# Kernel optimization log

Hardware: AMD Instinct MI355X
Metric: run time of the kernel (lower is better)

Reference implementation:

```python
import jax, jax.numpy as jnp
import numpy as np
from jax import lax

N, E, H = 100000, 768, 1024   # candidates, span-emb dim, FFNN hidden
K, A = 1500, 50               # top-k mentions, max antecedents
NUM_DOCS = 10

def _ffnn(x, w0, b0, w1, b1, w2, b2):
    h = jax.nn.relu(x @ w0 + b0)
    h = jax.nn.relu(h @ w1 + b1)
    return (h @ w2 + b2)[..., 0]

def setup_inputs() -> dict:
    key = jax.random.key(0)
    ks = jax.random.split(key, 8)
    emb = jax.random.normal(ks[0], (N, E), dtype=jnp.float32)
    doc_ids = jnp.sort(jax.random.randint(ks[1], (N,), 0, NUM_DOCS))
    def w(k, shape):
        fan_in = shape[0]
        return jax.random.normal(k, shape, dtype=jnp.float32) / np.sqrt(fan_in)
    return {
        'candidate_span_emb': emb,
        'candidate_doc_ids': doc_ids,
        'uw0': w(ks[2], (E, H)), 'ub0': jnp.zeros((H,), jnp.float32),
        'uw1': w(ks[3], (H, H)), 'ub1': jnp.zeros((H,), jnp.float32),
        'uw2': w(ks[4], (H, 1)), 'ub2': jnp.zeros((1,), jnp.float32),
        'pw0': w(ks[5], (3 * E, H)), 'pb0': jnp.zeros((H,), jnp.float32),
        'pw1': w(ks[6], (H, H)), 'pb1': jnp.zeros((H,), jnp.float32),
        'pw2': w(ks[7], (H, 1)), 'pb2': jnp.zeros((1,), jnp.float32),
    }

def reference(candidate_span_emb, candidate_doc_ids,
              uw0, ub0, uw1, ub1, uw2, ub2,
              pw0, pb0, pw1, pb1, pw2, pb2):
    # 1) unary mention scores over all candidate spans  [N]
    scores = _ffnn(candidate_span_emb, uw0, ub0, uw1, ub1, uw2, ub2)
    # 2) top-k span pruning (extract_spans with sort_spans=True -> sorted ids)
    _, top_idx = lax.top_k(scores, K)
    top_idx = jnp.sort(top_idx)
    mention_emb = candidate_span_emb[top_idx]          # [K, E]
    mention_scores = scores[top_idx]                   # [K]
    mention_doc_ids = candidate_doc_ids[top_idx]       # [K]
    # 3) antecedent index construction + doc-boundary mask
    raw = jnp.arange(K)[:, None] - (jnp.arange(A) + 1)[None, :]   # [K, A]
    antecedents = jnp.maximum(raw, 0)
    mask = (mention_doc_ids[:, None] == mention_doc_ids[antecedents]) & (raw >= 0)
    log_mask = jnp.where(mask, 0.0, -jnp.inf).astype(jnp.float32)
    # 4) pairwise antecedent scoring: [m, a, m*a] -> FFNN + unary terms
    ante_emb = mention_emb[antecedents]                 # [K, A, E]
    tgt = jnp.broadcast_to(mention_emb[:, None, :], (K, A, E))
    pair_emb = jnp.concatenate([tgt, ante_emb, tgt * ante_emb], axis=-1)  # [K, A, 3E]
    pair_scores = _ffnn(pair_emb, pw0, pb0, pw1, pb1, pw2, pb2)           # [K, A]
    ante_scores = pair_scores + mention_scores[:, None] + mention_scores[antecedents]
    # 5) dummy antecedent column prepended
    out = jnp.concatenate([jnp.zeros((K, 1), jnp.float32), ante_scores + log_mask], axis=1)
    return out  # [K, A+1]
```

## Files before the change

### kernel.cpp

```cpp
#include <hip/hip_runtime.h>
#include <cstdint>
#include <cstddef>

#define NC 100000
#define ED 768
#define HD 1024
#define KTOP 1500
#define AA 50
#define NPAIR (KTOP*AA)
#define PSTRIDE 100096
#define PSLICES 8

typedef __attribute__((ext_vector_type(8))) short v8s;
typedef __attribute__((ext_vector_type(4))) float f32x4;

__device__ __forceinline__ float relu_(float x){ return fmaxf(x, 0.f); }
__device__ __forceinline__ float bf2f(ushort h){ return __uint_as_float(((unsigned)h) << 16); }
__device__ __forceinline__ ushort f2b(float f){
    unsigned u = __float_as_uint(f);
    return (ushort)((u + 0x7fffu + ((u >> 16) & 1u)) >> 16);
}
__device__ __forceinline__ unsigned pack2(float a, float b){
    return (unsigned)f2b(a) | ((unsigned)f2b(b) << 16);
}
__device__ __forceinline__ unsigned fkey(float s){
    unsigned u = __float_as_uint(s);
    return (u & 0x80000000u) ? ~u : (u | 0x80000000u);
}
__device__ __forceinline__ float sanitize_(float v)
{
    unsigned bu = __float_as_uint(v);
    if ((bu & 0x7f800000u) == 0x7f800000u)
        v = (bu & 0x007fffffu) ? 0.f : ((bu >> 31) ? -3.0e38f : 3.0e38f);
    return v;
}

#define AS1(p) ((const __attribute__((address_space(1))) void*)(p))
#define AS3(p) ((__attribute__((address_space(3))) void*)(p))

template<int EPI>
__global__ __launch_bounds__(256, 4)
void bgemm_k(const ushort* __restrict__ A, int lda,
             const ushort* __restrict__ BT, int ldb,
             void* __restrict__ Cv, int ldc, int M, int Ksz, int MP,
             const float* __restrict__ bias,
             const float* __restrict__ Ub, const float* __restrict__ Vb, int p0,
             const float* __restrict__ w2, float* __restrict__ partS)
{
    const int bid = blockIdx.x;
    const int xcd = bid & 7;
    const int i0  = bid >> 3;
    const int np  = i0 & 7;
    const int bmp = ((i0 >> 3) << 3) + xcd;
    if (bmp >= MP) return;
    const int bm = bmp << 7;
    const int bn = np << 7;

    __shared__ __align__(16) ushort Al[128*64];
    __shared__ __align__(16) ushort Bl[128*64];
    __shared__ float srow[2][128];
    const int t = threadIdx.x;
    const int l = t & 63;
    const int w = t >> 6;
    const int wr = (w >> 1) << 6;
    const int wc = (w & 1) << 6;
    const int r15 = l & 15, q4 = l >> 4;
    const int srow8 = l >> 3;
    const int schnk = l & 7;

    f32x4 acc[4][4];
#pragma unroll
    for (int r = 0; r < 4; ++r)
#pragma unroll
        for (int c = 0; c < 4; ++c) acc[r][c] = (f32x4){0.f,0.f,0.f,0.f};

    for (int k0 = 0; k0 < Ksz; k0 += 64) {
        __syncthreads();
#pragma unroll
        for (int q = 0; q < 4; ++q) {
            int rbase = w*32 + q*8;
            int row = rbase + srow8;
            int cs = schnk ^ (row & 7);
            int gr = bm + row; if (gr > M-1) gr = M-1;
            __builtin_amdgcn_global_load_lds(AS1(A + (size_t)gr*lda + k0 + cs*8),
                                             AS3(Al + rbase*64), 16, 0, 0);
            int gn = bn + row;
            __builtin_amdgcn_global_load_lds(AS1(BT + (size_t)gn*ldb + k0 + cs*8),
                                             AS3(Bl + rbase*64), 16, 0, 0);
        }
        __syncthreads();
#pragma unroll
        for (int ks = 0; ks < 2; ++ks) {
            const int clin = ks*4 + q4;
            v8s af[4], bf[4];
#pragma unroll
            for (int r = 0; r < 4; ++r) {
                int row = wr + r*16 + r15;
                af[r] = *(const v8s*)(Al + row*64 + ((clin ^ (row & 7))*8));
                int col = wc + r*16 + r15;
                bf[r] = *(const v8s*)(Bl + col*64 + ((clin ^ (col & 7))*8));
            }
#pragma unroll
            for (int r = 0; r < 4; ++r)
#pragma unroll
                for (int c = 0; c < 4; ++c)
                    acc[r][c] = __builtin_amdgcn_mfma_f32_16x16x32_bf16(bf[c], af[r], acc[r][c], 0, 0, 0);
        }
    }

    if (EPI == 4) {
        float sacc[4];
#pragma unroll
        for (int r = 0; r < 4; ++r) sacc[r] = 0.f;
#pragma unroll
        for (int c = 0; c < 4; ++c) {
            int n0 = bn + wc + c*16 + q4*4;
            const float4 bb = *(const float4*)(bias + n0);
            const float4 ww = *(const float4*)(w2 + n0);
#pragma unroll
            for (int r = 0; r < 4; ++r) {
                sacc[r] = fmaf(relu_(acc[r][c][0] + bb.x), ww.x, sacc[r]);
                sacc[r] = fmaf(relu_(acc[r][c][1] + bb.y), ww.y, sacc[r]);
                sacc[r] = fmaf(relu_(acc[r][c][2] + bb.z), ww.z, sacc[r]);
                sacc[r] = fmaf(relu_(acc[r][c][3] + bb.w), ww.w, sacc[r]);
            }
        }
        __syncthreads();
        srow[t >> 7][t & 127] = 0.f;
        __syncthreads();
#pragma unroll
        for (int r = 0; r < 4; ++r) {
            float s = sacc[r];
            s += __shfl_xor(s, 16, 64);
            s += __shfl_xor(s, 32, 64);
            if (q4 == 0) srow[w & 1][wr + r*16 + r15] = s;
        }
        __syncthreads();
        if (t < 128) {
            int m = bm + t;
            if (m < M) partS[(size_t)np*PSTRIDE + m] = srow[0][t] + srow[1][t];
        }
    } else {
        float*  Cf = (float*)Cv;
        ushort* Cb = (ushort*)Cv;
#pragma unroll
        for (int r = 0; r < 4; ++r) {
            int m = bm + wr + r*16 + r15;
            if (m >= M) continue;
            int iu = 0, iv = 0;
            if (EPI == 3) {
                int p = p0 + m;
                iu = p / 50;
                int a = p - iu*50;
                iv = iu - a - 1; if (iv < 0) iv = 0;
            }
#pragma unroll
            for (int c = 0; c < 4; ++c) {
                int n0 = bn + wc + c*16 + q4*4;
                float x0 = acc[r][c][0], x1 = acc[r][c][1];
                float x2 = acc[r][c][2], x3 = acc[r][c][3];
                if (EPI == 0) {
                    float4 o; o.x=x0; o.y=x1; o.z=x2; o.w=x3;
                    *(float4*)(Cf + (size_t)m*ldc + n0) = o;
                } else if (EPI == 1) {
                    const float4 bb = *(const float4*)(bias + n0);
                    float4 o; o.x=x0+bb.x; o.y=x1+bb.y; o.z=x2+bb.z; o.w=x3+bb.w;
                    *(float4*)(Cf + (size_t)m*ldc + n0) = o;
                } else if (EPI == 2) {
                    const float4 bb = *(const float4*)(bias + n0);
                    uint2 o;
                    o.x = pack2(relu_(x0+bb.x), relu_(x1+bb.y));
                    o.y = pack2(relu_(x2+bb.z), relu_(x3+bb.w));
                    *(uint2*)(Cb + (size_t)m*ldc + n0) = o;
                } else {
                    const float4 uu = *(const float4*)(Ub + (size_t)iu*HD + n0);
                    const float4 vv = *(const float4*)(Vb + (size_t)iv*HD + n0);
                    uint2 o;
                    o.x = pack2(relu_(x0+uu.x+vv.x), relu_(x1+uu.y+vv.y));
                    o.y = pack2(relu_(x2+uu.z+vv.z), relu_(x3+uu.w+vv.w));
                    *(uint2*)(Cb + (size_t)m*ldc + n0) = o;
                }
            }
        }
    }
}

__global__ void comb_k(const float* __restrict__ part, const float* __restrict__ b2,
                       float* __restrict__ out, int M)
{
    int i = blockIdx.x*256 + threadIdx.x;
    if (i < M) {
        float s = b2[0];
#pragma unroll
        for (int p = 0; p < PSLICES; ++p) s += part[(size_t)p*PSTRIDE + i];
        out[i] = s;
    }
}

__global__ void conv_k(const float* __restrict__ src, ushort* __restrict__ dst, int n4)
{
    for (int x = blockIdx.x*blockDim.x + threadIdx.x; x < n4; x += gridDim.x*blockDim.x) {
        float4 v = ((const float4*)src)[x];
        ushort4 o; o.x = f2b(v.x); o.y = f2b(v.y); o.z = f2b(v.z); o.w = f2b(v.w);
        ((ushort4*)dst)[x] = o;
    }
}

__global__ __launch_bounds__(256)
void wt_k(const float* __restrict__ W, ushort* __restrict__ WT, int K, int N)
{
    __shared__ float ld[32][33];
    int tx = threadIdx.x & 31, ty = threadIdx.x >> 5;
    int k0 = blockIdx.y*32, n0 = blockIdx.x*32;
#pragma unroll
    for (int r = 0; r < 4; ++r)
        ld[ty + r*8][tx] = W[(size_t)(k0 + ty + r*8)*N + n0 + tx];
    __syncthreads();
#pragma unroll
    for (int r = 0; r < 4; ++r)
        WT[(size_t)(n0 + ty + r*8)*K + k0 + tx] = f2b(ld[tx][ty + r*8]);
}

__global__ void init_sel_k(unsigned* state, unsigned* hist, int* top, int ntop)
{
    int t = threadIdx.x;
    if (t < 64) state[t] = 0u;
    for (int i = t; i < 1024; i += 256) hist[i] = 0u;
    for (int k = t; k < ntop; k += 256) top[k] = k;
}

__global__ __launch_bounds__(256)
void hist_k(const float* __restrict__ scores, int N, unsigned* __restrict__ hist,
            const unsigned* __restrict__ state, int shift)
{
    __shared__ unsigned lh[256];
    lh[threadIdx.x] = 0u;
    __syncthreads();
    unsigned prefix = state[0];
    for (int i = blockIdx.x*blockDim.x + threadIdx.x; i < N; i += gridDim.x*blockDim.x) {
        unsigned u = fkey(scores[i]);
        bool ok = (shift == 24) || ((u >> (shift+8)) == prefix);
        if (ok) atomicAdd(&lh[(u >> shift) & 0xffu], 1u);
    }
    __syncthreads();
    unsigned c = lh[threadIdx.x];
    if (c) atomicAdd(&hist[threadIdx.x], c);
}

__global__ void select_k(const unsigned* __restrict__ hist, unsigned* state, int shift, int K)
{
    if (threadIdx.x != 0) return;
    unsigned P = state[1];
    unsigned acc = 0; int bstar = 0;
    for (int b = 255; b >= 0; --b) {
        unsigned h = hist[b];
        if (P + acc + h >= (unsigned)K) { bstar = b; break; }
        acc += h;
    }
    state[0] = (shift == 24) ? (unsigned)bstar : ((state[0] << 8) | (unsigned)bstar);
    state[1] = P + acc;
    if (shift == 0) state[2] = state[0];
}

__global__ __launch_bounds__(256)
void cnt_k(const float* __restrict__ scores, int N, const unsigned* __restrict__ state,
           unsigned* __restrict__ gt_cnt, unsigned* __restrict__ eq_cnt)
{
    unsigned ut = state[2];
    int base = blockIdx.x * 2048;
    unsigned g = 0, e = 0;
    for (int q = 0; q < 8; ++q) {
        int i = base + q*256 + threadIdx.x;
        if (i < N) { unsigned u = fkey(scores[i]); g += (u > ut); e += (u == ut); }
    }
    __shared__ unsigned sg[256], se[256];
    sg[threadIdx.x] = g; se[threadIdx.x] = e;
    __syncthreads();
    for (int s = 128; s > 0; s >>= 1) {
        if (threadIdx.x < s) { sg[threadIdx.x] += sg[threadIdx.x+s]; se[threadIdx.x] += se[threadIdx.x+s]; }
        __syncthreads();
    }
    if (threadIdx.x == 0) { gt_cnt[blockIdx.x] = sg[0]; eq_cnt[blockIdx.x] = se[0]; }
}

__global__ void scan_k(const unsigned* gt_cnt, const unsigned* eq_cnt,
                       unsigned* gt_off, unsigned* eq_off, int nblk, unsigned* state, int K)
{
    if (threadIdx.x != 0) return;
    unsigned ag = 0, ae = 0;
    for (int b = 0; b < nblk; ++b) {
        gt_off[b] = ag; eq_off[b] = ae;
        ag += gt_cnt[b]; ae += eq_cnt[b];
    }
    state[3] = ag;
    state[4] = ag < (unsigned)K ? (unsigned)K - ag : 0u;
}

__global__ __launch_bounds__(256)
void write_k(const float* __restrict__ scores, int N, const unsigned* __restrict__ state,
             const unsigned* __restrict__ gt_off, const unsigned* __restrict__ eq_off,
             int* __restrict__ top_idx, int Ksel)
{
    unsigned ut = state[2], T = state[4];
    int base = blockIdx.x * 2048;
    unsigned grun = gt_off[blockIdx.x], erun = eq_off[blockIdx.x];
    __shared__ unsigned wg[4], we[4];
    int t = threadIdx.x, lane = t & 63, wv = t >> 6;
    for (int q = 0; q < 8; ++q) {
        int i = base + q*256 + t;
        bool valid = i < N;
        unsigned u = valid ? fkey(scores[i]) : 0u;
        bool g = valid && (u > ut);
        bool e = valid && (u == ut);
        unsigned long long bg = __ballot(g), be = __ballot(e);
        unsigned long long lt = (1ull << lane) - 1ull;
        unsigned lpg = __popcll(bg & lt), lpe = __popcll(be & lt);
        if (lane == 0) { wg[wv] = (unsigned)__popcll(bg); we[wv] = (unsigned)__popcll(be); }
        __syncthreads();
        unsigned bsg = 0, bse = 0, tg = 0, te = 0;
        for (int ww = 0; ww < 4; ++ww) {
            if (ww < wv) { bsg += wg[ww]; bse += we[ww]; }
            tg += wg[ww]; te += we[ww];
        }
        unsigned grank = grun + bsg + lpg;
        unsigned erank = erun + bse + lpe;
        unsigned pos = 0xffffffffu;
        if (g)                   pos = grank + (erank < T ? erank : T);
        else if (e && erank < T) pos = grank + erank;
        if (pos < (unsigned)Ksel) top_idx[pos] = i;
        grun += tg; erun += te;
        __syncthreads();
    }
}

__global__ void gatherF_k(const float* __restrict__ emb, const int* __restrict__ doc,
                          const int* __restrict__ topA, const float* __restrict__ scores,
                          ushort* __restrict__ meb, float* __restrict__ ms,
                          int* __restrict__ mdoc)
{
    int k = blockIdx.x;
    int idx = topA[k]; if (idx < 0 || idx >= NC) idx = 0;
    int t = threadIdx.x;
    if (t < 192) {
        float4 v = ((const float4*)(emb + (size_t)idx*ED))[t];
        ushort4 o; o.x = f2b(v.x); o.y = f2b(v.y); o.z = f2b(v.z); o.w = f2b(v.w);
        *(ushort4*)(meb + (size_t)k*ED + t*4) = o;
    }
    if (t == 192) { ms[k] = scores[idx]; mdoc[k] = doc[idx]; }
}

__global__ __launch_bounds__(256)
void prodb_k(const ushort* __restrict__ meb, ushort* __restrict__ prod, int p0, int C)
{
    int tot = C * 96;
    for (int x = blockIdx.x*blockDim.x + threadIdx.x; x < tot; x += gridDim.x*blockDim.x) {
        int pc = x / 96, e = x - pc*96;
        int p = p0 + pc;
        int i = p / 50, a = p - i*50;
        int j = i - a - 1; if (j < 0) j = 0;
        uint4 ui = ((const uint4*)(meb + (size_t)i*ED))[e];
        uint4 uj = ((const uint4*)(meb + (size_t)j*ED))[e];
        auto pk = [](unsigned a_, unsigned b_) -> unsigned {
            float lo = bf2f((ushort)(a_ & 0xffffu)) * bf2f((ushort)(b_ & 0xffffu));
            float hi = bf2f((ushort)(a_ >> 16))     * bf2f((ushort)(b_ >> 16));
            return (unsigned)f2b(lo) | ((unsigned)f2b(hi) << 16);
        };
        uint4 o; o.x = pk(ui.x, uj.x); o.y = pk(ui.y, uj.y);
                 o.z = pk(ui.z, uj.z); o.w = pk(ui.w, uj.w);
        ((uint4*)(prod + (size_t)pc*ED))[e] = o;
    }
}

__global__ __launch_bounds__(256)
void assemble_k(const float* __restrict__ ps, const float* __restrict__ ms,
                const int* __restrict__ mdoc, float* __restrict__ out)
{
    int idx = blockIdx.x*blockDim.x + threadIdx.x;
    if (idx >= KTOP*(AA+1)) return;
    int i = idx / (AA+1), col = idx - i*(AA+1);
    if (col == 0) { out[idx] = 0.f; return; }
    int a = col - 1;
    int raw = i - a - 1;
    int j = raw < 0 ? 0 : raw;
    bool mk = (raw >= 0) && (mdoc[i] == mdoc[j]);
    float v = mk ? (ps[i*AA + a] + ms[i] + ms[j]) : -3.0e38f;
    out[idx] = sanitize_(v);
}

static inline int swz_grid(int MP) { return ((MP + 7) & ~7) * 8; }

extern "C" void kernel_launch(void* const* d_in, const int* in_sizes, int n_in,
                              void* d_out, int out_size, void* d_ws, size_t ws_size,
                              hipStream_t stream)
{
    const float* emb = (const float*)d_in[0];
    const int*   doc = (const int*)d_in[1];
    const float* uw0 = (const float*)d_in[2];
    const float* ub0 = (const float*)d_in[3];
    const float* uw1 = (const float*)d_in[4];
    const float* ub1 = (const float*)d_in[5];
    const float* uw2 = (const float*)d_in[6];
    const float* ub2 = (const float*)d_in[7];
    const float* pw0 = (const float*)d_in[8];
    const float* pb0 = (const float*)d_in[9];
    const float* pw1 = (const float*)d_in[10];
    const float* pb1 = (const float*)d_in[11];
    const float* pw2 = (const float*)d_in[12];
    const float* pb2 = (const float*)d_in[13];
    float* out = (float*)d_out;

    char* ws = (char*)d_ws;
    size_t off = 0;
    auto alloc = [&](size_t bytes) -> void* {
        void* p = ws + off;
        off = (off + bytes + 255) & ~(size_t)255;
        return p;
    };
    const int NBLKA = (NC + 2047) / 2048;
    float*    scoresA = (float*)alloc((size_t)NC*4);
    float*    partS   = (float*)alloc((size_t)PSLICES*PSTRIDE*4);
    unsigned* stateA  = (unsigned*)alloc(64*4);
    unsigned* histA   = (unsigned*)alloc(1024*4);
    unsigned* gtA  = (unsigned*)alloc((size_t)NBLKA*4);
    unsigned* eqA  = (unsigned*)alloc((size_t)NBLKA*4);
    unsigned* gtoA = (unsigned*)alloc((size_t)NBLKA*4);
    unsigned* eqoA = (unsigned*)alloc((size_t)NBLKA*4);
    int*      topA = (int*)alloc((size_t)KTOP*4);
    ushort*   meb  = (ushort*)alloc((size_t)KTOP*ED*2);
    float*    ms   = (float*)alloc((size_t)KTOP*4);
    int*      mdoc = (int*)alloc((size_t)KTOP*4);
    float*    U    = (float*)alloc((size_t)KTOP*HD*4);
    float*    V    = (float*)alloc((size_t)KTOP*HD*4);
    float*    ps   = (float*)alloc((size_t)NPAIR*4);
    ushort*   uw0T = (ushort*)alloc((size_t)HD*ED*2);
    ushort*   uw1T = (ushort*)alloc((size_t)HD*HD*2);
    ushort*   paT  = (ushort*)alloc((size_t)HD*ED*2);
    ushort*   pbT  = (ushort*)alloc((size_t)HD*ED*2);
    ushort*   pcT  = (ushort*)alloc((size_t)HD*ED*2);
    ushort*   pw1T = (ushort*)alloc((size_t)HD*HD*2);
    size_t fixed = off;
    size_t avail = ws_size > fixed ? ws_size - fixed : 0;

    wt_k<<<dim3(HD/32, ED/32), 256, 0, stream>>>(uw0, uw0T, ED, HD);
    wt_k<<<dim3(HD/32, HD/32), 256, 0, stream>>>(uw1, uw1T, HD, HD);
    wt_k<<<dim3(HD/32, ED/32), 256, 0, stream>>>(pw0, paT, ED, HD);
    wt_k<<<dim3(HD/32, ED/32), 256, 0, stream>>>(pw0 + (size_t)ED*HD, pbT, ED, HD);
    wt_k<<<dim3(HD/32, ED/32), 256, 0, stream>>>(pw0 + (size_t)2*ED*HD, pcT, ED, HD);
    wt_k<<<dim3(HD/32, HD/32), 256, 0, stream>>>(pw1, pw1T, HD, HD);

    {
        long Rl = (long)(avail / 3584);
        int R = (int)(Rl > 100096 ? 100096 : Rl);
        R &= ~127; if (R < 128) R = 128;
        ushort* embB = (ushort*)(ws + fixed);
        ushort* H1b  = embB + (size_t)R*ED;
        for (int r0 = 0; r0 < NC; r0 += R) {
            int rows = NC - r0 < R ? NC - r0 : R;
            int MP = (rows + 127)/128;
            conv_k<<<1024, 256, 0, stream>>>(emb + (size_t)r0*ED, embB, rows*192);
            bgemm_k<2><<<swz_grid(MP), 256, 0, stream>>>(embB, ED, uw0T, ED, H1b, HD,
                rows, ED, MP, ub0, nullptr, nullptr, 0, nullptr, nullptr);
            bgemm_k<4><<<swz_grid(MP), 256, 0, stream>>>(H1b, HD, uw1T, HD, nullptr, 0,
                rows, HD, MP, ub1, nullptr, nullptr, 0, uw2, partS);
            comb_k<<<(rows + 255)/256, 256, 0, stream>>>(partS, ub2, scoresA + r0, rows);
        }
    }

    init_sel_k<<<1, 256, 0, stream>>>(stateA, histA, topA, KTOP);
    for (int pass = 0; pass < 4; ++pass) {
        int shift = 24 - pass*8;
        hist_k<<<256, 256, 0, stream>>>(scoresA, NC, histA + pass*256, stateA, shift);
        select_k<<<1, 64, 0, stream>>>(histA + pass*256, stateA, shift, KTOP);
    }
    cnt_k<<<NBLKA, 256, 0, stream>>>(scoresA, NC, stateA, gtA, eqA);
    scan_k<<<1, 64, 0, stream>>>(gtA, eqA, gtoA, eqoA, NBLKA, stateA, KTOP);
    write_k<<<NBLKA, 256, 0, stream>>>(scoresA, NC, stateA, gtoA, eqoA, topA, KTOP);
    gatherF_k<<<KTOP, 256, 0, stream>>>(emb, doc, topA, scoresA, meb, ms, mdoc);

    {
        int MP = (KTOP + 127)/128;
        bgemm_k<1><<<swz_grid(MP), 256, 0, stream>>>(meb, ED, paT, ED, U, HD, KTOP, ED,
            MP, pb0, nullptr, nullptr, 0, nullptr, nullptr);
        bgemm_k<0><<<swz_grid(MP), 256, 0, stream>>>(meb, ED, pbT, ED, V, HD, KTOP, ED,
            MP, nullptr, nullptr, nullptr, 0, nullptr, nullptr);
    }

    {
        long Cl = (long)(avail / 3584);
        int Cp = (int)(Cl > NPAIR ? NPAIR : Cl);
        Cp &= ~127; if (Cp < 128) Cp = 128;
        ushort* prodb = (ushort*)(ws + fixed);
        ushort* h0b = prodb + (size_t)Cp*ED;
        for (int p0 = 0; p0 < NPAIR; p0 += Cp) {
            int pc = NPAIR - p0 < Cp ? NPAIR - p0 : Cp;
            int MP = (pc + 127)/128;
            prodb_k<<<1024, 256, 0, stream>>>(meb, prodb, p0, pc);
            bgemm_k<3><<<swz_grid(MP), 256, 0, stream>>>(prodb, ED, pcT, ED, h0b, HD,
                pc, ED, MP, nullptr, U, V, p0, nullptr, nullptr);
            bgemm_k<4><<<swz_grid(MP), 256, 0, stream>>>(h0b, HD, pw1T, HD, nullptr, 0,
                pc, HD, MP, pb1, nullptr, nullptr, 0, pw2, partS);
            comb_k<<<(pc + 255)/256, 256, 0, stream>>>(partS, pb2, ps + p0, pc);
        }
    }

    assemble_k<<<(KTOP*(AA+1) + 255)/256, 256, 0, stream>>>(ps, ms, mdoc, out);
}
```

Measured before the change: 1.021 ms.

## Compact valid antecedent pairs and skip FFNN work on masked pairs

Adds a count, scan and write pass that builds a compacted index list of antecedent pairs that are valid: a non-negative antecedent index in the same document. The pair product construction and both pairwise GEMMs then run only over those compacted rows, with the effective row count read on the device. The combine step scatters scores back to their original pair positions. This removes GEMM work for pairs whose output is forced to -inf by the mask. In exchange it adds three small kernels and an indirect index load. Masked score slots are now left unwritten, which is only safe if the assemble step ignores them rather than adding -inf to leftover values.

```diff
diff --git a/kernel.cpp b/kernel.cpp
--- a/kernel.cpp
+++ b/kernel.cpp
@@ -8,6 +8,7 @@
 #define KTOP 1500
 #define AA 50
 #define NPAIR (KTOP*AA)
+#define NBLKP ((NPAIR + 2047) / 2048)
 #define PSTRIDE 100096
 #define PSLICES 8
 
@@ -45,7 +46,8 @@
              void* __restrict__ Cv, int ldc, int M, int Ksz, int MP,
              const float* __restrict__ bias,
              const float* __restrict__ Ub, const float* __restrict__ Vb, int p0,
-             const float* __restrict__ w2, float* __restrict__ partS)
+             const float* __restrict__ w2, float* __restrict__ partS,
+             const int* __restrict__ cntp, const int* __restrict__ pidx)
 {
     const int bid = blockIdx.x;
     const int xcd = bid & 7;
@@ -53,7 +55,14 @@
     const int np  = i0 & 7;
     const int bmp = ((i0 >> 3) << 3) + xcd;
     if (bmp >= MP) return;
+    int Meff = M;
+    if (cntp) {
+        int c = *cntp - p0;
+        if (c < Meff) Meff = c;
+        if (Meff <= 0) return;
+    }
     const int bm = bmp << 7;
+    if (bm >= Meff) return;
     const int bn = np << 7;
 
     __shared__ __align__(16) ushort Al[128*64];
@@ -81,7 +90,7 @@
             int rbase = w*32 + q*8;
             int row = rbase + srow8;
             int cs = schnk ^ (row & 7);
-            int gr = bm + row; if (gr > M-1) gr = M-1;
+            int gr = bm + row; if (gr > Meff-1) gr = Meff-1;
             __builtin_amdgcn_global_load_lds(AS1(A + (size_t)gr*lda + k0 + cs*8),
                                              AS3(Al + rbase*64), 16, 0, 0);
             int gn = bn + row;
@@ -138,7 +147,7 @@
         __syncthreads();
         if (t < 128) {
             int m = bm + t;
-            if (m < M) partS[(size_t)np*PSTRIDE + m] = srow[0][t] + srow[1][t];
+            if (m < Meff) partS[(size_t)np*PSTRIDE + m] = srow[0][t] + srow[1][t];
         }
     } else {
         float*  Cf = (float*)Cv;
@@ -146,10 +155,10 @@
 #pragma unroll
         for (int r = 0; r < 4; ++r) {
             int m = bm + wr + r*16 + r15;
-            if (m >= M) continue;
+            if (m >= Meff) continue;
             int iu = 0, iv = 0;
             if (EPI == 3) {
-                int p = p0 + m;
+                int p = pidx[p0 + m];
                 iu = p / 50;
                 int a = p - iu*50;
                 iv = iu - a - 1; if (iv < 0) iv = 0;
@@ -197,6 +206,20 @@
     }
 }
 
+__global__ void combp_k(const float* __restrict__ part, const float* __restrict__ b2,
+                        float* __restrict__ ps, int Cp, int p0,
+                        const int* __restrict__ cntp, const int* __restrict__ pidx)
+{
+    int i = blockIdx.x*256 + threadIdx.x;
+    int Meff = *cntp - p0; if (Meff > Cp) Meff = Cp;
+    if (i < Meff) {
+        float s = b2[0];
+#pragma unroll
+        for (int p = 0; p < PSLICES; ++p) s += part[(size_t)p*PSTRIDE + i];
+        ps[pidx[p0 + i]] = s;
+    }
+}
+
 __global__ void conv_k(const float* __restrict__ src, ushort* __restrict__ dst, int n4)
 {
     for (int x = blockIdx.x*blockDim.x + threadIdx.x; x < n4; x += gridDim.x*blockDim.x) {
@@ -349,13 +372,78 @@
     if (t == 192) { ms[k] = scores[idx]; mdoc[k] = doc[idx]; }
 }
 
-__global__ __launch_bounds__(256)
-void prodb_k(const ushort* __restrict__ meb, ushort* __restrict__ prod, int p0, int C)
-{
-    int tot = C * 96;
+__device__ __forceinline__ bool pvalid_(int p, const int* __restrict__ mdoc)
+{
+    int i = p / 50, a = p - i*50;
+    int j = i - a - 1;
+    return (j >= 0) && (mdoc[i] == mdoc[j]);
+}
+
+__global__ __launch_bounds__(256)
+void pcnt_k(const int* __restrict__ mdoc, unsigned* __restrict__ blk_cnt)
+{
+    int base = blockIdx.x * 2048;
+    unsigned c = 0;
+    for (int q = 0; q < 8; ++q) {
+        int p = base + q*256 + threadIdx.x;
+        if (p < NPAIR && pvalid_(p, mdoc)) ++c;
+    }
+    __shared__ unsigned sc[256];
+    sc[threadIdx.x] = c;
+    __syncthreads();
+    for (int s = 128; s > 0; s >>= 1) {
+        if (threadIdx.x < s) sc[threadIdx.x] += sc[threadIdx.x + s];
+        __syncthreads();
+    }
+    if (threadIdx.x == 0) blk_cnt[blockIdx.x] = sc[0];
+}
+
+__global__ void pscan_k(const unsigned* __restrict__ blk_cnt,
+                        unsigned* __restrict__ blk_off, int* __restrict__ pcnt)
+{
+    if (threadIdx.x != 0) return;
+    unsigned a = 0;
+    for (int b = 0; b < NBLKP; ++b) { blk_off[b] = a; a += blk_cnt[b]; }
+    pcnt[0] = (int)a;
+}
+
+__global__ __launch_bounds__(256)
+void pwrite_k(const int* __restrict__ mdoc, const unsigned* __restrict__ blk_off,
+              int* __restrict__ pidx)
+{
+    int base = blockIdx.x * 2048;
+    unsigned run = blk_off[blockIdx.x];
+    __shared__ unsigned wcnt[4];
+    int t = threadIdx.x, lane = t & 63, wv = t >> 6;
+    for (int q = 0; q < 8; ++q) {
+        int p = base + q*256 + t;
+        bool v = (p < NPAIR) && pvalid_(p, mdoc);
+        unsigned long long bv = __ballot(v);
+        unsigned long long lt = (1ull << lane) - 1ull;
+        unsigned lp = __popcll(bv & lt);
+        if (lane == 0) wcnt[wv] = (unsigned)__popcll(bv);
+        __syncthreads();
+        unsigned bs = 0, tot = 0;
+        for (int ww = 0; ww < 4; ++ww) {
+            if (ww < wv) bs += wcnt[ww];
+            tot += wcnt[ww];
+        }
+        if (v) pidx[run + bs + lp] = p;
+        run += tot;
+        __syncthreads();
+    }
+}
+
+__global__ __launch_bounds__(256)
+void prodb_k(const ushort* __restrict__ meb, ushort* __restrict__ prod, int p0, int Cp,
+             const int* __restrict__ cntp, const int* __restrict__ pidx)
+{
+    int Meff = *cntp - p0; if (Meff > Cp) Meff = Cp;
+    if (Meff <= 0) return;
+    int tot = Meff * 96;
     for (int x = blockIdx.x*blockDim.x + threadIdx.x; x < tot; x += gridDim.x*blockDim.x) {
         int pc = x / 96, e = x - pc*96;
-        int p = p0 + pc;
+        int p = pidx[p0 + pc];
         int i = p / 50, a = p - i*50;
         int j = i - a - 1; if (j < 0) j = 0;
         uint4 ui = ((const uint4*)(meb + (size_t)i*ED))[e];
@@ -432,6 +520,10 @@
     float*    U    = (float*)alloc((size_t)KTOP*HD*4);
     float*    V    = (float*)alloc((size_t)KTOP*HD*4);
     float*    ps   = (float*)alloc((size_t)NPAIR*4);
+    unsigned* pbc  = (unsigned*)alloc((size_t)NBLKP*4);
+    unsigned* pbo  = (unsigned*)alloc((size_t)NBLKP*4);
+    int*      pcnt = (int*)alloc(256);
+    int*      pidx = (int*)alloc((size_t)NPAIR*4);
     ushort*   uw0T = (ushort*)alloc((size_t)HD*ED*2);
     ushort*   uw1T = (ushort*)alloc((size_t)HD*HD*2);
     ushort*   paT  = (ushort*)alloc((size_t)HD*ED*2);
@@ -459,9 +551,11 @@
             int MP = (rows + 127)/128;
             conv_k<<<1024, 256, 0, stream>>>(emb + (size_t)r0*ED, embB, rows*192);
             bgemm_k<2><<<swz_grid(MP), 256, 0, stream>>>(embB, ED, uw0T, ED, H1b, HD,
-                rows, ED, MP, ub0, nullptr, nullptr, 0, nullptr, nullptr);
+                rows, ED, MP, ub0, nullptr, nullptr, 0, nullptr, nullptr,
+                nullptr, nullptr);
             bgemm_k<4><<<swz_grid(MP), 256, 0, stream>>>(H1b, HD, uw1T, HD, nullptr, 0,
-                rows, HD, MP, ub1, nullptr, nullptr, 0, uw2, partS);
+                rows, HD, MP, ub1, nullptr, nullptr, 0, uw2, partS,
+                nullptr, nullptr);
             comb_k<<<(rows + 255)/256, 256, 0, stream>>>(partS, ub2, scoresA + r0, rows);
         }
     }
@@ -477,12 +571,16 @@
     write_k<<<NBLKA, 256, 0, stream>>>(scoresA, NC, stateA, gtoA, eqoA, topA, KTOP);
     gatherF_k<<<KTOP, 256, 0, stream>>>(emb, doc, topA, scoresA, meb, ms, mdoc);
 
+    pcnt_k<<<NBLKP, 256, 0, stream>>>(mdoc, pbc);
+    pscan_k<<<1, 64, 0, stream>>>(pbc, pbo, pcnt);
+    pwrite_k<<<NBLKP, 256, 0, stream>>>(mdoc, pbo, pidx);
+
     {
         int MP = (KTOP + 127)/128;
         bgemm_k<1><<<swz_grid(MP), 256, 0, stream>>>(meb, ED, paT, ED, U, HD, KTOP, ED,
-            MP, pb0, nullptr, nullptr, 0, nullptr, nullptr);
+            MP, pb0, nullptr, nullptr, 0, nullptr, nullptr, nullptr, nullptr);
         bgemm_k<0><<<swz_grid(MP), 256, 0, stream>>>(meb, ED, pbT, ED, V, HD, KTOP, ED,
-            MP, nullptr, nullptr, nullptr, 0, nullptr, nullptr);
+            MP, nullptr, nullptr, nullptr, 0, nullptr, nullptr, nullptr, nullptr);
     }
 
     {
@@ -494,12 +592,13 @@
         for (int p0 = 0; p0 < NPAIR; p0 += Cp) {
             int pc = NPAIR - p0 < Cp ? NPAIR - p0 : Cp;
             int MP = (pc + 127)/128;
-            prodb_k<<<1024, 256, 0, stream>>>(meb, prodb, p0, pc);
+            prodb_k<<<1024, 256, 0, stream>>>(meb, prodb, p0, pc, pcnt, pidx);
             bgemm_k<3><<<swz_grid(MP), 256, 0, stream>>>(prodb, ED, pcT, ED, h0b, HD,
-                pc, ED, MP, nullptr, U, V, p0, nullptr, nullptr);
+                pc, ED, MP, nullptr, U, V, p0, nullptr, nullptr, pcnt, pidx);
             bgemm_k<4><<<swz_grid(MP), 256, 0, stream>>>(h0b, HD, pw1T, HD, nullptr, 0,
-                pc, HD, MP, pb1, nullptr, nullptr, 0, pw2, partS);
-            comb_k<<<(pc + 255)/256, 256, 0, stream>>>(partS, pb2, ps + p0, pc);
+                pc, HD, MP, pb1, nullptr, nullptr, p0, pw2, partS, pcnt, nullptr);
+            combp_k<<<(pc + 255)/256, 256, 0, stream>>>(partS, pb2, ps, pc, p0,
+                                                        pcnt, pidx);
         }
     }
 
```

Result: faster. 913.8 us, median of 2 (-10.5%).
